# Performance work log

Measured on AMD Instinct MI355X. Metric: run time of the kernel, lower is better.

The kernel has to match this reference:

```python
import jax, jax.numpy as jnp
import numpy as np

N = 4096        # num_pbits
STEPS = 16384   # sequential single-spin updates (4 sweeps)
BETA = 1.0


def setup_inputs() -> dict:
    key = jax.random.key(0)
    k1, k2, k3, k4 = jax.random.split(key, 4)
    # random_graph: symmetric, zero-diagonal, nonnegative weights; maxcut_J = -W
    U = jax.random.uniform(k1, (N, N), dtype=jnp.float32)
    Wu = jnp.triu(U, 1)
    J = -(Wu + Wu.T)
    h = jnp.zeros((N,), dtype=jnp.float32)
    # initial spins in {-1, +1}
    m0 = jnp.sign(jax.random.normal(k2, (N,), dtype=jnp.float32))
    m0 = jnp.where(m0 == 0, 1.0, m0)
    # pre-drawn per-step RNG: update index and uniform noise in [0,1)
    idx = jax.random.randint(k3, (STEPS,), 0, N, dtype=jnp.int32)
    u = jax.random.uniform(k4, (STEPS,), dtype=jnp.float32)
    return {"J": J, "h": h, "m0": m0, "idx": idx, "u": u}


def reference(J, h, m0, idx, u):
    # Sequential Glauber single p-bit updates (continuous noise).
    def step(m, xs):
        i, ui = xs
        I_i = jnp.dot(J[i], m) + h[i]          # local field, [scalar]
        p_i = jnp.tanh(BETA * I_i)
        r = 2.0 * ui - 1.0                      # uniform in [-1, 1)
        s = jnp.sign(p_i - r)
        s = jnp.where(s == 0, jnp.float32(1.0), s)
        return m.at[i].set(s), None

    m, _ = jax.lax.scan(step, m0, (idx, u))
    return m
```

## Files before the change

### kernel.cpp

```cpp
#include <hip/hip_runtime.h>
#include <math.h>

#define N 4096
#define STEPS 16384
#define WIN 32
#define NWIN (STEPS / WIN)
#define MBLK 1024
#define SBS 36

__device__ __forceinline__ void lgkm_barrier() {
  asm volatile("s_waitcnt lgkmcnt(0)\n\ts_barrier" ::: "memory");
}

__global__ __launch_bounds__(256) void pre_kernel(const float* __restrict__ u,
                                                  const int* __restrict__ idx,
                                                  double* __restrict__ thr,
                                                  int* __restrict__ lastocc) {
  int t = blockIdx.x * 256 + threadIdx.x;
  if (t < STEPS) {
    float r = 2.0f * u[t] - 1.0f;
    double rd = (double)r;
    thr[t] = 0.5 * log((1.0 + rd) / (1.0 - rd));
    int cbase = t & ~(WIN - 1);
    int my = idx[t];
    int lo = 1;
    for (int tt = (t & (WIN - 1)) + 1; tt < WIN; ++tt)
      if (idx[cbase + tt] == my) { lo = 0; break; }
    lastocc[t] = lo;
  }
}

__global__ __launch_bounds__(256) void init_field_kernel(const float* __restrict__ J,
                                                         const float* __restrict__ h,
                                                         const float* __restrict__ m0,
                                                         double* __restrict__ I) {
  __shared__ double red[256];
  int row = blockIdx.x;
  const float4* Jr = (const float4*)(J + (size_t)row * N);
  const float4* mv = (const float4*)m0;
  double acc = 0.0;
  for (int q = threadIdx.x; q < N / 4; q += 256) {
    float4 a = Jr[q];
    float4 b = mv[q];
    acc += (double)(a.x * b.x) + (double)(a.y * b.y) +
           (double)(a.z * b.z) + (double)(a.w * b.w);
  }
  red[threadIdx.x] = acc;
  __syncthreads();
  for (int s = 128; s > 0; s >>= 1) {
    if (threadIdx.x < s) red[threadIdx.x] += red[threadIdx.x + s];
    __syncthreads();
  }
  if (threadIdx.x == 0) I[row] = red[0] + (double)h[row];
}

__global__ __launch_bounds__(MBLK) void pbit_kernel(const float* __restrict__ J,
                                                    const float* __restrict__ m0,
                                                    const int* __restrict__ idx,
                                                    const double* __restrict__ thr,
                                                    const int* __restrict__ lastocc,
                                                    const double* __restrict__ I0,
                                                    float* __restrict__ out) {
  __shared__ __align__(16) double field_lds[N];
  __shared__ __align__(16) float m_lds[N];
  __shared__ __align__(16) float ST_lds[WIN * SBS];
  __shared__ __align__(16) int   pubi_lds[WIN];
  __shared__ __align__(16) float pubd_lds[WIN];
  __shared__ int pubF_lds;

  const int tid = threadIdx.x;

  double i0, i1, i2, i3;
  {
    const double* ip = I0 + 4 * tid;
    i0 = ip[0]; i1 = ip[1]; i2 = ip[2]; i3 = ip[3];
    *(double2*)(field_lds + 4 * tid + 0) = make_double2(i0, i1);
    *(double2*)(field_lds + 4 * tid + 2) = make_double2(i2, i3);
  }
  ((float4*)m_lds)[tid] = ((const float4*)m0)[tid];

  const int t32 = tid & 31;
  const int jrow = tid >> 1;
  const int half = (tid & 1) * 16;

  int mi = 0, ni = 0, mlo = 0, nlo = 0;
  double mt = 0.0, nt = 0.0;

  if (tid < 64) {
    mi = idx[t32];       mt = thr[t32];       mlo = lastocc[t32];
    ni = idx[WIN + t32]; nt = thr[WIN + t32]; nlo = lastocc[WIN + t32];
    int r0 = __shfl(mi, jrow);
    const float* Jr = J + (size_t)r0 * N;
#pragma unroll
    for (int q = 0; q < 16; ++q) {
      int c = __shfl(mi, half + q);
      ST_lds[jrow * SBS + half + q] = Jr[c];
    }
  }
  __syncthreads();

  for (int k = 0; k < NWIN; ++k) {
    if (tid < 64) {
      int growv = __shfl(ni, jrow);
      const float* Jg = J + (size_t)growv * N;
      int gc0  = __shfl(ni, half + 0),  gc1  = __shfl(ni, half + 1);
      int gc2  = __shfl(ni, half + 2),  gc3  = __shfl(ni, half + 3);
      int gc4  = __shfl(ni, half + 4),  gc5  = __shfl(ni, half + 5);
      int gc6  = __shfl(ni, half + 6),  gc7  = __shfl(ni, half + 7);
      int gc8  = __shfl(ni, half + 8),  gc9  = __shfl(ni, half + 9);
      int gc10 = __shfl(ni, half + 10), gc11 = __shfl(ni, half + 11);
      int gc12 = __shfl(ni, half + 12), gc13 = __shfl(ni, half + 13);
      int gc14 = __shfl(ni, half + 14), gc15 = __shfl(ni, half + 15);
      float gv0  = Jg[gc0],  gv1  = Jg[gc1],  gv2  = Jg[gc2],  gv3  = Jg[gc3];
      float gv4  = Jg[gc4],  gv5  = Jg[gc5],  gv6  = Jg[gc6],  gv7  = Jg[gc7];
      float gv8  = Jg[gc8],  gv9  = Jg[gc9],  gv10 = Jg[gc10], gv11 = Jg[gc11];
      float gv12 = Jg[gc12], gv13 = Jg[gc13], gv14 = Jg[gc14], gv15 = Jg[gc15];
      int b2 = (k + 2) * WIN; if (b2 >= STEPS) b2 = 0;
      int n2i = idx[b2 + t32];
      double n2t = thr[b2 + t32];
      int n2lo = lastocc[b2 + t32];
      const float* sp = &ST_lds[(size_t)t32 * SBS];
      float4 s0 = *(const float4*)(sp + 0),  s1 = *(const float4*)(sp + 4);
      float4 s2 = *(const float4*)(sp + 8),  s3 = *(const float4*)(sp + 12);
      float4 s4 = *(const float4*)(sp + 16), s5 = *(const float4*)(sp + 20);
      float4 s6 = *(const float4*)(sp + 24), s7 = *(const float4*)(sp + 28);
      double Ival = field_lds[mi];
      float mcur = m_lds[mi];
      float finals = 0.0f, finald = 0.0f;
      int conf = -1;
      bool locked = false;
      while (true) {
        float s = (Ival >= mt) ? 1.0f : -1.0f;
        float dl = s - mcur;
        unsigned long long mask = __ballot(dl != 0.0f) & 0xFFFFFFFFull;
        mask &= (~0ull) << (conf + 1);
        if (mask == 0) {
          if (!locked) { finals = s; finald = 0.0f; }
          break;
        }
        int f = (int)__builtin_ctzll(mask);
        if (!locked && t32 <= f) { finals = s; finald = dl; locked = true; }
        float dl_f = __int_as_float(__builtin_amdgcn_readlane(__float_as_int(dl), f));
        float s_f  = __int_as_float(__builtin_amdgcn_readlane(__float_as_int(s), f));
        int   i_f  = __builtin_amdgcn_readlane(mi, f);
        float4 sel;
        switch (f >> 2) {
          case 0: sel = s0; break; case 1: sel = s1; break;
          case 2: sel = s2; break; case 3: sel = s3; break;
          case 4: sel = s4; break; case 5: sel = s5; break;
          case 6: sel = s6; break; default: sel = s7; break;
        }
        float xcol;
        switch (f & 3) {
          case 0: xcol = sel.x; break; case 1: xcol = sel.y; break;
          case 2: xcol = sel.z; break; default: xcol = sel.w; break;
        }
        Ival += (double)(xcol * dl_f);
        if (mi == i_f) mcur = s_f;
        conf = f;
      }
      unsigned long long fm = __ballot((tid < WIN) && (finald != 0.0f));
      if (tid < WIN) {
        if (finald != 0.0f) {
          int pos = __popcll(fm & ((1ull << t32) - 1ull));
          pubi_lds[pos] = mi;
          pubd_lds[pos] = finald;
        }
        if (mlo) m_lds[mi] = finals;
        if (tid == 0) pubF_lds = (int)__popcll(fm);
      }
      {
        float* dst = &ST_lds[jrow * SBS + half];
        *(float4*)(dst + 0)  = make_float4(gv0, gv1, gv2, gv3);
        *(float4*)(dst + 4)  = make_float4(gv4, gv5, gv6, gv7);
        *(float4*)(dst + 8)  = make_float4(gv8, gv9, gv10, gv11);
        *(float4*)(dst + 12) = make_float4(gv12, gv13, gv14, gv15);
      }
      mi = ni;  mt = nt;  mlo = nlo;
      ni = n2i; nt = n2t; nlo = n2lo;
    }
    lgkm_barrier();

    {
      int F = pubF_lds;
      if (F > 0) {
        const float* Jb = J + 4 * (size_t)tid;
#pragma unroll
        for (int b = 0; b < WIN; b += 8) {
          if (b < F) {
            int4 r1 = *(const int4*)(pubi_lds + b);
            int4 r2 = *(const int4*)(pubi_lds + b + 4);
            float4 d1 = *(const float4*)(pubd_lds + b);
            float4 d2 = *(const float4*)(pubd_lds + b + 4);
            int rr[8] = {r1.x, r1.y, r1.z, r1.w, r2.x, r2.y, r2.z, r2.w};
            float dd[8] = {d1.x, d1.y, d1.z, d1.w, d2.x, d2.y, d2.z, d2.w};
            float4 rv[8];
#pragma unroll
            for (int t = 0; t < 8; ++t)
              if (b + t < F) rv[t] = *(const float4*)(Jb + (size_t)rr[t] * N);
            float a0 = 0.f, a1 = 0.f, a2 = 0.f, a3 = 0.f;
#pragma unroll
            for (int t = 0; t < 8; ++t)
              if (b + t < F) {
                a0 += rv[t].x * dd[t]; a1 += rv[t].y * dd[t];
                a2 += rv[t].z * dd[t]; a3 += rv[t].w * dd[t];
              }
            i0 += (double)a0; i1 += (double)a1;
            i2 += (double)a2; i3 += (double)a3;
          }
        }
        *(double2*)(field_lds + 4 * tid + 0) = make_double2(i0, i1);
        *(double2*)(field_lds + 4 * tid + 2) = make_double2(i2, i3);
      }
    }
    lgkm_barrier();
  }

  __syncthreads();
  ((float4*)out)[tid] = ((const float4*)m_lds)[tid];
}

extern "C" void kernel_launch(void* const* d_in, const int* in_sizes, int n_in,
                              void* d_out, int out_size, void* d_ws, size_t ws_size,
                              hipStream_t stream) {
  const float* J = (const float*)d_in[0];
  const float* h = (const float*)d_in[1];
  const float* m0 = (const float*)d_in[2];
  const int* idx = (const int*)d_in[3];
  const float* u = (const float*)d_in[4];
  float* out = (float*)d_out;

  double* thr = (double*)d_ws;
  double* I0 = (double*)((char*)d_ws + STEPS * sizeof(double));
  int* lastocc = (int*)((char*)d_ws + STEPS * sizeof(double)
                                    + N * sizeof(double));

  pre_kernel<<<dim3(STEPS / 256), dim3(256), 0, stream>>>(u, idx, thr, lastocc);
  init_field_kernel<<<dim3(N), dim3(256), 0, stream>>>(J, h, m0, I0);
  pbit_kernel<<<dim3(1), dim3(MBLK), 0, stream>>>(J, m0, idx, thr, lastocc, I0, out);
}
```

Baseline: 1.955 ms.

## Resolve window spin flips in batches using stability bounds instead of one flip per iteration

Result: slower. 2.285 ms (+16.9%).

```diff
diff --git a/kernel.cpp b/kernel.cpp
--- a/kernel.cpp
+++ b/kernel.cpp
@@ -15,7 +15,7 @@
 __global__ __launch_bounds__(256) void pre_kernel(const float* __restrict__ u,
                                                   const int* __restrict__ idx,
                                                   double* __restrict__ thr,
-                                                  int* __restrict__ lastocc) {
+                                                  int* __restrict__ samemask) {
   int t = blockIdx.x * 256 + threadIdx.x;
   if (t < STEPS) {
     float r = 2.0f * u[t] - 1.0f;
@@ -23,10 +23,10 @@
     thr[t] = 0.5 * log((1.0 + rd) / (1.0 - rd));
     int cbase = t & ~(WIN - 1);
     int my = idx[t];
-    int lo = 1;
-    for (int tt = (t & (WIN - 1)) + 1; tt < WIN; ++tt)
-      if (idx[cbase + tt] == my) { lo = 0; break; }
-    lastocc[t] = lo;
+    unsigned int sm = 0u;
+    for (int q = 0; q < WIN; ++q)
+      if (idx[cbase + q] == my) sm |= (1u << q);
+    samemask[t] = (int)sm;
   }
 }
 
@@ -58,7 +58,7 @@
                                                     const float* __restrict__ m0,
                                                     const int* __restrict__ idx,
                                                     const double* __restrict__ thr,
-                                                    const int* __restrict__ lastocc,
+                                                    const int* __restrict__ samemask,
                                                     const double* __restrict__ I0,
                                                     float* __restrict__ out) {
   __shared__ __align__(16) double field_lds[N];
@@ -83,12 +83,13 @@
   const int jrow = tid >> 1;
   const int half = (tid & 1) * 16;
 
-  int mi = 0, ni = 0, mlo = 0, nlo = 0;
+  int mi = 0, ni = 0;
+  unsigned int msm = 0u, nsm = 0u;
   double mt = 0.0, nt = 0.0;
 
   if (tid < 64) {
-    mi = idx[t32];       mt = thr[t32];       mlo = lastocc[t32];
-    ni = idx[WIN + t32]; nt = thr[WIN + t32]; nlo = lastocc[WIN + t32];
+    mi = idx[t32];       mt = thr[t32];       msm = (unsigned int)samemask[t32];
+    ni = idx[WIN + t32]; nt = thr[WIN + t32]; nsm = (unsigned int)samemask[WIN + t32];
     int r0 = __shfl(mi, jrow);
     const float* Jr = J + (size_t)r0 * N;
 #pragma unroll
@@ -118,46 +119,55 @@
       int b2 = (k + 2) * WIN; if (b2 >= STEPS) b2 = 0;
       int n2i = idx[b2 + t32];
       double n2t = thr[b2 + t32];
-      int n2lo = lastocc[b2 + t32];
+      unsigned int n2sm = (unsigned int)samemask[b2 + t32];
       const float* sp = &ST_lds[(size_t)t32 * SBS];
       float4 s0 = *(const float4*)(sp + 0),  s1 = *(const float4*)(sp + 4);
       float4 s2 = *(const float4*)(sp + 8),  s3 = *(const float4*)(sp + 12);
       float4 s4 = *(const float4*)(sp + 16), s5 = *(const float4*)(sp + 20);
       float4 s6 = *(const float4*)(sp + 24), s7 = *(const float4*)(sp + 28);
       double Ival = field_lds[mi];
-      float mcur = m_lds[mi];
+      float mycur = m_lds[mi];
+      const unsigned int below = (1u << t32) - 1u;
       float finals = 0.0f, finald = 0.0f;
-      int conf = -1;
-      bool locked = false;
+      unsigned int rem = 0xFFFFFFFFu;
       while (true) {
-        float s = (Ival >= mt) ? 1.0f : -1.0f;
-        float dl = s - mcur;
-        unsigned long long mask = __ballot(dl != 0.0f) & 0xFFFFFFFFull;
-        mask &= (~0ull) << (conf + 1);
-        if (mask == 0) {
-          if (!locked) { finals = s; finald = 0.0f; }
+        bool sup = (Ival >= mt);
+        float s = sup ? 1.0f : -1.0f;
+        unsigned int D  = (unsigned int)__ballot(sup);
+        unsigned int FL = (unsigned int)__ballot(s != mycur) & rem;
+        if (FL == 0u) {
+          if ((rem >> t32) & 1u) { finals = s; finald = 0.0f; }
           break;
         }
-        int f = (int)__builtin_ctzll(mask);
-        if (!locked && t32 <= f) { finals = s; finald = dl; locked = true; }
-        float dl_f = __int_as_float(__builtin_amdgcn_readlane(__float_as_int(dl), f));
-        float s_f  = __int_as_float(__builtin_amdgcn_readlane(__float_as_int(s), f));
-        int   i_f  = __builtin_amdgcn_readlane(mi, f);
-        float4 sel;
-        switch (f >> 2) {
-          case 0: sel = s0; break; case 1: sel = s1; break;
-          case 2: sel = s2; break; case 3: sel = s3; break;
-          case 4: sel = s4; break; case 5: sel = s5; break;
-          case 6: sel = s6; break; default: sel = s7; break;
-        }
-        float xcol;
-        switch (f & 3) {
-          case 0: xcol = sel.x; break; case 1: xcol = sel.y; break;
-          case 2: xcol = sel.z; break; default: xcol = sel.w; break;
-        }
-        Ival += (double)(xcol * dl_f);
-        if (mi == i_f) mcur = s_f;
-        conf = f;
+        unsigned int FLb = FL & below;
+        int nb = __popc(FLb);
+        bool stable = (nb == 0) || (fabs(Ival - mt) > (double)(2 * nb));
+        bool safe = (FLb & msm) == 0u;
+        unsigned int good = (unsigned int)__ballot(stable && safe);
+        unsigned int bad = rem & ~good;
+        unsigned int pm = bad ? ((1u << __builtin_ctz(bad)) - 1u) : 0xFFFFFFFFu;
+        unsigned int fin = rem & pm;
+        unsigned int batch = FL & pm;
+        if ((fin >> t32) & 1u) {
+          finals = s;
+          finald = (s != mycur) ? (2.0f * s) : 0.0f;
+        }
+        float delta = 0.0f;
+#define APQ(q, rq) { float dq = ((batch >> (q)) & 1u) ? (((D >> (q)) & 1u) ? 2.0f : -2.0f) : 0.0f; \
+                     delta += (rq) * dq; }
+        APQ(0,  s0.x) APQ(1,  s0.y) APQ(2,  s0.z) APQ(3,  s0.w)
+        APQ(4,  s1.x) APQ(5,  s1.y) APQ(6,  s1.z) APQ(7,  s1.w)
+        APQ(8,  s2.x) APQ(9,  s2.y) APQ(10, s2.z) APQ(11, s2.w)
+        APQ(12, s3.x) APQ(13, s3.y) APQ(14, s3.z) APQ(15, s3.w)
+        APQ(16, s4.x) APQ(17, s4.y) APQ(18, s4.z) APQ(19, s4.w)
+        APQ(20, s5.x) APQ(21, s5.y) APQ(22, s5.z) APQ(23, s5.w)
+        APQ(24, s6.x) APQ(25, s6.y) APQ(26, s6.z) APQ(27, s6.w)
+        APQ(28, s7.x) APQ(29, s7.y) APQ(30, s7.z) APQ(31, s7.w)
+#undef APQ
+        Ival += (double)delta;
+        if (__popc(batch & msm) & 1) mycur = -mycur;
+        rem &= ~pm;
+        if (rem == 0u) break;
       }
       unsigned long long fm = __ballot((tid < WIN) && (finald != 0.0f));
       if (tid < WIN) {
@@ -166,6 +176,7 @@
           pubi_lds[pos] = mi;
           pubd_lds[pos] = finald;
         }
+        bool mlo = (msm & (0xFFFFFFFEu << t32)) == 0u;
         if (mlo) m_lds[mi] = finals;
         if (tid == 0) pubF_lds = (int)__popcll(fm);
       }
@@ -176,8 +187,8 @@
         *(float4*)(dst + 8)  = make_float4(gv8, gv9, gv10, gv11);
         *(float4*)(dst + 12) = make_float4(gv12, gv13, gv14, gv15);
       }
-      mi = ni;  mt = nt;  mlo = nlo;
-      ni = n2i; nt = n2t; nlo = n2lo;
+      mi = ni;  mt = nt;  msm = nsm;
+      ni = n2i; nt = n2t; nsm = n2sm;
     }
     lgkm_barrier();
 
@@ -232,10 +243,10 @@
 
   double* thr = (double*)d_ws;
   double* I0 = (double*)((char*)d_ws + STEPS * sizeof(double));
-  int* lastocc = (int*)((char*)d_ws + STEPS * sizeof(double)
-                                    + N * sizeof(double));
-
-  pre_kernel<<<dim3(STEPS / 256), dim3(256), 0, stream>>>(u, idx, thr, lastocc);
+  int* samemask = (int*)((char*)d_ws + STEPS * sizeof(double)
+                                     + N * sizeof(double));
+
+  pre_kernel<<<dim3(STEPS / 256), dim3(256), 0, stream>>>(u, idx, thr, samemask);
   init_field_kernel<<<dim3(N), dim3(256), 0, stream>>>(J, h, m0, I0);
-  pbit_kernel<<<dim3(1), dim3(MBLK), 0, stream>>>(J, m0, idx, thr, lastocc, I0, out);
-}
+  pbit_kernel<<<dim3(1), dim3(MBLK), 0, stream>>>(J, m0, idx, thr, samemask, I0, out);
+}
```
